# Kernel tuning notes

Measured on AMD Instinct MI355X. Metric: run time of the kernel, lower is better.

## Reference

```python
import jax, jax.numpy as jnp
import numpy as np

B, S, E, H, BS = 4, 4096, 1024, 1024, 128  # batch, seq, embed, head_size, block_size


def setup_inputs() -> dict:
    key = jax.random.key(0)
    k1, k2, k3, k4 = jax.random.split(key, 4)
    x = jax.random.normal(k1, (B, S, E), dtype=jnp.float32)
    W_qkv = jax.random.normal(k2, (E, 3 * H), dtype=jnp.float32) * (E ** -0.5)
    W_out = jax.random.normal(k3, (H, H), dtype=jnp.float32) * (H ** -0.5)
    b_out = jax.random.normal(k4, (H,), dtype=jnp.float32) * 0.01
    return {"x": x, "W_qkv": W_qkv, "W_out": W_out, "b_out": b_out}


def reference(x, W_qkv, W_out, b_out):
    b, s, e = x.shape
    h = W_out.shape[1]
    nb = s // BS  # number of blocks (block-diagonal attention)
    qkv = x @ W_qkv                      # [B, S, 3H]
    q, k, v = jnp.split(qkv, 3, axis=-1)

    def blk(t):
        return t.reshape(b, nb, BS, h)   # [B, nb, BS, H]

    scale = h ** -0.5
    # each query block attends only its own key/value block
    scores = jnp.einsum('bnqd,bnkd->bnqk', blk(q), blk(k)) * scale  # [B, nb, BS, BS]
    causal = jnp.tril(jnp.ones((BS, BS), dtype=bool))  # diagonal block of full tril
    scores = jnp.where(causal, scores, -jnp.inf)
    scores = scores - jnp.max(scores, axis=-1, keepdims=True)
    p = jnp.exp(scores)
    p = p / (jnp.sum(p, axis=-1, keepdims=True) + 1e-6)  # faithful: softmax with +1e-6 eps
    out = jnp.einsum('bnqk,bnkd->bnqd', p, blk(v)).reshape(b, s, h)
    return out @ W_out.T + b_out
```

## Files before the change

### kernel.cpp

```cpp
#include <hip/hip_runtime.h>
#include <hip/hip_bf16.h>

typedef __attribute__((ext_vector_type(8))) short short8;
typedef __attribute__((ext_vector_type(4))) float float4_;

__device__ __forceinline__ short f2b(float f) {
  union { __hip_bfloat16 h; short s; } u;
  u.h = __float2bfloat16(f);
  return u.s;
}
__device__ __forceinline__ float b2f(short s) {
  union { short s; __hip_bfloat16 h; } u;
  u.s = s;
  return __bfloat162float(u.h);
}
__device__ __forceinline__ short8 cvt8(float4_ lo, float4_ hi) {
  short8 r;
#pragma unroll
  for (int t = 0; t < 4; t++) { r[t] = f2b(lo[t]); r[t + 4] = f2b(hi[t]); }
  return r;
}

__global__ __launch_bounds__(256) void f32_to_b16(
    const float* __restrict__ in, short* __restrict__ out, long n)
{
  const long i = ((long)blockIdx.x * 256 + threadIdx.x) * 8;
  if (i >= n) return;
  float4_ lo = *(const float4_*)&in[i];
  float4_ hi = *(const float4_*)&in[i + 4];
  *(short8*)&out[i] = cvt8(lo, hi);
}

__global__ __launch_bounds__(256) void transpose64(
    const float* __restrict__ in, short* __restrict__ out, int R, int C)
{
  __shared__ __align__(16) short T[64 * 72];
  const int tid = threadIdx.x;
  const int r0 = blockIdx.y * 64;
  const int c0 = blockIdx.x * 64;
  const int r  = tid >> 2;
  const int cp = (tid & 3) * 16;
#pragma unroll
  for (int g = 0; g < 4; g++) {
    float4_ v = *(const float4_*)&in[(long)(r0 + r) * C + c0 + cp + g * 4];
#pragma unroll
    for (int t = 0; t < 4; t++) T[(cp + g * 4 + t) * 72 + r] = f2b(v[t]);
  }
  __syncthreads();
  const int c  = tid >> 2;
  const int rp = (tid & 3) * 16;
  short8 w0 = *(const short8*)&T[c * 72 + rp];
  short8 w1 = *(const short8*)&T[c * 72 + rp + 8];
  *(short8*)&out[(long)(c0 + c) * R + r0 + rp] = w0;
  *(short8*)&out[(long)(c0 + c) * R + r0 + rp + 8] = w1;
}

__global__ __launch_bounds__(256) void gemm_bt(
    const void* __restrict__ Av, int lda, int a_f32,
    const short* __restrict__ B,
    void* __restrict__ Cv, int ldc, int c_f32,
    int K, const float* __restrict__ bias)
{
  __shared__ __align__(16) short As[128 * 32];
  __shared__ __align__(16) short Bs[128 * 32];
  const int tid  = threadIdx.x;
  const int lane = tid & 63;
  const int w    = tid >> 6;
  const int quad = lane >> 4;
  const int l15  = lane & 15;
  const int wm   = (w >> 1) * 64;
  const int wn   = (w & 1) * 64;
  const int m0   = blockIdx.y * 128;
  const int n0   = blockIdx.x * 128;

  float4_ acc[4][4] = {};

  const int srow = tid >> 2;
  const int kp   = (tid & 3) * 8;

  for (int k0 = 0; k0 < K; k0 += 32) {
    short8 a_lo, a_hi;
    if (a_f32) {
      const float* Af = (const float*)Av;
      float4_ l0 = *(const float4_*)&Af[(long)(m0 + srow) * lda + k0 + kp];
      float4_ l1 = *(const float4_*)&Af[(long)(m0 + srow) * lda + k0 + kp + 4];
      float4_ h0 = *(const float4_*)&Af[(long)(m0 + srow + 64) * lda + k0 + kp];
      float4_ h1 = *(const float4_*)&Af[(long)(m0 + srow + 64) * lda + k0 + kp + 4];
      a_lo = cvt8(l0, l1);
      a_hi = cvt8(h0, h1);
    } else {
      const short* As_ = (const short*)Av;
      a_lo = *(const short8*)&As_[(long)(m0 + srow) * lda + k0 + kp];
      a_hi = *(const short8*)&As_[(long)(m0 + srow + 64) * lda + k0 + kp];
    }
    short8 b_lo = *(const short8*)&B[(long)(n0 + srow) * K + k0 + kp];
    short8 b_hi = *(const short8*)&B[(long)(n0 + srow + 64) * K + k0 + kp];
    __syncthreads();
    *(short8*)&As[srow * 32 + kp]        = a_lo;
    *(short8*)&As[(srow + 64) * 32 + kp] = a_hi;
    *(short8*)&Bs[srow * 32 + kp]        = b_lo;
    *(short8*)&Bs[(srow + 64) * 32 + kp] = b_hi;
    __syncthreads();
    short8 a[4], b[4];
#pragma unroll
    for (int i = 0; i < 4; i++)
      a[i] = *(const short8*)&As[(wm + i * 16 + l15) * 32 + quad * 8];
#pragma unroll
    for (int j = 0; j < 4; j++)
      b[j] = *(const short8*)&Bs[(wn + j * 16 + l15) * 32 + quad * 8];
#pragma unroll
    for (int i = 0; i < 4; i++)
#pragma unroll
      for (int j = 0; j < 4; j++)
        acc[i][j] = __builtin_amdgcn_mfma_f32_16x16x32_bf16(a[i], b[j], acc[i][j], 0, 0, 0);
  }

#pragma unroll
  for (int i = 0; i < 4; i++) {
    const int rm = m0 + wm + i * 16 + quad * 4;
#pragma unroll
    for (int j = 0; j < 4; j++) {
      const int cn = n0 + wn + j * 16 + l15;
      if (c_f32) {
        float* C = (float*)Cv;
        const float bv = bias ? bias[cn] : 0.0f;
#pragma unroll
        for (int r = 0; r < 4; r++)
          C[(long)(rm + r) * ldc + cn] = acc[i][j][r] + bv;
      } else {
        short* C = (short*)Cv;
#pragma unroll
        for (int r = 0; r < 4; r++)
          C[(long)(rm + r) * ldc + cn] = f2b(acc[i][j][r]);
      }
    }
  }
}

__global__ __launch_bounds__(256) void attn_blockdiag(short* __restrict__ qkv)
{
  __shared__ __align__(16) short Qs[128 * 32];
  __shared__ __align__(16) short Ks[128 * 32];
  __shared__ __align__(16) short Ps[128 * 136];

  const int tid  = threadIdx.x;
  const int lane = tid & 63;
  const int w    = tid >> 6;
  const int quad = lane >> 4;
  const int l15  = lane & 15;
  const long base = (long)blockIdx.x * 128 * 3072;

  float4_ acc[2][8] = {};
  const int srow = tid >> 2;
  const int kp   = (tid & 3) * 8;
  const short* Qg = qkv + base;
  const short* Kg = qkv + base + 1024;

  for (int k0 = 0; k0 < 1024; k0 += 32) {
    short8 q_lo = *(const short8*)&Qg[(long)srow * 3072 + k0 + kp];
    short8 q_hi = *(const short8*)&Qg[(long)(srow + 64) * 3072 + k0 + kp];
    short8 k_lo = *(const short8*)&Kg[(long)srow * 3072 + k0 + kp];
    short8 k_hi = *(const short8*)&Kg[(long)(srow + 64) * 3072 + k0 + kp];
    __syncthreads();
    *(short8*)&Qs[srow * 32 + kp]        = q_lo;
    *(short8*)&Qs[(srow + 64) * 32 + kp] = q_hi;
    *(short8*)&Ks[srow * 32 + kp]        = k_lo;
    *(short8*)&Ks[(srow + 64) * 32 + kp] = k_hi;
    __syncthreads();
    short8 a0 = *(const short8*)&Qs[(w * 32 + l15) * 32 + quad * 8];
    short8 a1 = *(const short8*)&Qs[(w * 32 + 16 + l15) * 32 + quad * 8];
#pragma unroll
    for (int j = 0; j < 8; j++) {
      short8 b = *(const short8*)&Ks[(j * 16 + l15) * 32 + quad * 8];
      acc[0][j] = __builtin_amdgcn_mfma_f32_16x16x32_bf16(a0, b, acc[0][j], 0, 0, 0);
      acc[1][j] = __builtin_amdgcn_mfma_f32_16x16x32_bf16(a1, b, acc[1][j], 0, 0, 0);
    }
  }
  __syncthreads();

  const float scale = 0.03125f;
#pragma unroll
  for (int i = 0; i < 2; i++) {
#pragma unroll
    for (int r = 0; r < 4; r++) {
      const int rowq = w * 32 + i * 16 + quad * 4 + r;
      float s[8];
      float mx = -3.0e38f;
#pragma unroll
      for (int j = 0; j < 8; j++) {
        const int col = j * 16 + l15;
        const float v = acc[i][j][r] * scale;
        s[j] = (col <= rowq) ? v : -3.0e38f;
        mx = fmaxf(mx, s[j]);
      }
      mx = fmaxf(mx, __shfl_xor(mx, 1));
      mx = fmaxf(mx, __shfl_xor(mx, 2));
      mx = fmaxf(mx, __shfl_xor(mx, 4));
      mx = fmaxf(mx, __shfl_xor(mx, 8));
      float p[8];
      float sum = 0.0f;
#pragma unroll
      for (int j = 0; j < 8; j++) {
        p[j] = (s[j] > -1.0e38f) ? __expf(s[j] - mx) : 0.0f;
        sum += p[j];
      }
      sum += __shfl_xor(sum, 1);
      sum += __shfl_xor(sum, 2);
      sum += __shfl_xor(sum, 4);
      sum += __shfl_xor(sum, 8);
      const float inv = 1.0f / (sum + 1e-6f);
#pragma unroll
      for (int j = 0; j < 8; j++)
        Ps[rowq * 136 + j * 16 + l15] = f2b(p[j] * inv);
    }
  }
  __syncthreads();

  const short* Vg = qkv + base + 2048;
  short* Op = qkv + base;
  for (int d0 = 0; d0 < 1024; d0 += 64) {
    float4_ o[2][4] = {};
#pragma unroll
    for (int kk = 0; kk < 4; kk++) {
      short8 a0 = *(const short8*)&Ps[(w * 32 + l15) * 136 + kk * 32 + quad * 8];
      short8 a1 = *(const short8*)&Ps[(w * 32 + 16 + l15) * 136 + kk * 32 + quad * 8];
      const int kb = kk * 32 + quad * 8;
#pragma unroll
      for (int j = 0; j < 4; j++) {
        const int d = d0 + j * 16 + l15;
        short8 b;
#pragma unroll
        for (int t = 0; t < 8; t++)
          b[t] = Vg[(long)(kb + t) * 3072 + d];
        o[0][j] = __builtin_amdgcn_mfma_f32_16x16x32_bf16(a0, b, o[0][j], 0, 0, 0);
        o[1][j] = __builtin_amdgcn_mfma_f32_16x16x32_bf16(a1, b, o[1][j], 0, 0, 0);
      }
    }
#pragma unroll
    for (int i = 0; i < 2; i++)
#pragma unroll
      for (int j = 0; j < 4; j++)
#pragma unroll
        for (int r = 0; r < 4; r++) {
          const int rq = w * 32 + i * 16 + quad * 4 + r;
          const int d  = d0 + j * 16 + l15;
          Op[(long)rq * 3072 + d] = f2b(o[i][j][r]);
        }
  }
}

extern "C" void kernel_launch(void* const* d_in, const int* in_sizes, int n_in,
                              void* d_out, int out_size, void* d_ws, size_t ws_size,
                              hipStream_t stream) {
  const float* x    = (const float*)d_in[0];
  const float* Wqkv = (const float*)d_in[1];
  const float* Wout = (const float*)d_in[2];
  const float* bout = (const float*)d_in[3];
  float* out = (float*)d_out;

  char* ws = (char*)d_ws;
  short* WqkvT = (short*)ws;
  short* Woutb = (short*)(ws + 6291456);
  short* qkv   = (short*)(ws + 8388608);
  short* xb    = (short*)(ws + 8388608 + (size_t)16384 * 3072 * 2);

  transpose64<<<dim3(48, 16), 256, 0, stream>>>(Wqkv, WqkvT, 1024, 3072);
  f32_to_b16<<<512, 256, 0, stream>>>(Wout, Woutb, 1048576L);

  if (ws_size >= 8388608 + (size_t)16384 * 3072 * 2 + (size_t)16384 * 1024 * 2) {
    f32_to_b16<<<8192, 256, 0, stream>>>(x, xb, 16777216L);
    gemm_bt<<<dim3(24, 128), 256, 0, stream>>>(xb, 1024, 0, WqkvT,
                                               qkv, 3072, 0, 1024, nullptr);
    attn_blockdiag<<<dim3(128), 256, 0, stream>>>(qkv);
    gemm_bt<<<dim3(8, 128), 256, 0, stream>>>(qkv, 3072, 0, Woutb,
                                              out, 1024, 1, 1024, bout);
  } else if (ws_size >= 8388608 + (size_t)16384 * 3072 * 2) {
    gemm_bt<<<dim3(24, 128), 256, 0, stream>>>(x, 1024, 1, WqkvT,
                                               qkv, 3072, 0, 1024, nullptr);
    attn_blockdiag<<<dim3(128), 256, 0, stream>>>(qkv);
    gemm_bt<<<dim3(8, 128), 256, 0, stream>>>(qkv, 3072, 0, Woutb,
                                              out, 1024, 1, 1024, bout);
  } else {
    for (int c = 0; c < 4; c++) {
      const float* xc = x + (long)c * 4096 * 1024;
      float* outc = out + (long)c * 4096 * 1024;
      gemm_bt<<<dim3(24, 32), 256, 0, stream>>>(xc, 1024, 1, WqkvT,
                                                qkv, 3072, 0, 1024, nullptr);
      attn_blockdiag<<<dim3(32), 256, 0, stream>>>(qkv);
      gemm_bt<<<dim3(8, 32), 256, 0, stream>>>(qkv, 3072, 0, Woutb,
                                               outc, 1024, 1, 1024, bout);
    }
  }
}
```

Measured before the change: 384.1 us.

## Split attention into QK-softmax and PV kernels, use async global-to-LDS loads

The single attention kernel, which ran only 128 blocks, is split into a QK+softmax kernel with 256 blocks (half a query block each) that writes P into the Q slot, and a PV kernel with 1024 blocks (one 128-column tile each) that writes output into the K slot. The final GEMM then reads from the K slot. The aim is to raise GPU occupancy on the attention stages, which previously used too few workgroups. GEMM and QK tile loads now use global_load_lds async copies instead of register staging. The separate x-to-bf16 conversion pass and the workspace-size fallbacks are dropped, so the GEMM converts fp32 x on the fly. This adds an extra round trip through global memory for P and assumes the larger workspace is always available.

```diff
diff --git a/kernel.cpp b/kernel.cpp
--- a/kernel.cpp
+++ b/kernel.cpp
@@ -3,16 +3,17 @@
 
 typedef __attribute__((ext_vector_type(8))) short short8;
 typedef __attribute__((ext_vector_type(4))) float float4_;
+
+__device__ __forceinline__ void async16(const void* g, void* l) {
+  __builtin_amdgcn_global_load_lds(
+      (const __attribute__((address_space(1))) unsigned int*)g,
+      (__attribute__((address_space(3))) unsigned int*)l, 16, 0, 0);
+}
 
 __device__ __forceinline__ short f2b(float f) {
   union { __hip_bfloat16 h; short s; } u;
   u.h = __float2bfloat16(f);
   return u.s;
-}
-__device__ __forceinline__ float b2f(short s) {
-  union { short s; __hip_bfloat16 h; } u;
-  u.s = s;
-  return __bfloat162float(u.h);
 }
 __device__ __forceinline__ short8 cvt8(float4_ lo, float4_ hi) {
   short8 r;
@@ -77,29 +78,27 @@
 
   const int srow = tid >> 2;
   const int kp   = (tid & 3) * 8;
+  char* AsW = (char*)As + w * 1024;
+  char* BsW = (char*)Bs + w * 1024;
+  const short* Bb0 = B + (long)(n0 + srow) * K;
+  const short* Bb1 = B + (long)(n0 + srow + 64) * K;
 
   for (int k0 = 0; k0 < K; k0 += 32) {
-    short8 a_lo, a_hi;
+    async16(Bb0 + k0 + kp, BsW);
+    async16(Bb1 + k0 + kp, BsW + 4096);
     if (a_f32) {
       const float* Af = (const float*)Av;
       float4_ l0 = *(const float4_*)&Af[(long)(m0 + srow) * lda + k0 + kp];
       float4_ l1 = *(const float4_*)&Af[(long)(m0 + srow) * lda + k0 + kp + 4];
       float4_ h0 = *(const float4_*)&Af[(long)(m0 + srow + 64) * lda + k0 + kp];
       float4_ h1 = *(const float4_*)&Af[(long)(m0 + srow + 64) * lda + k0 + kp + 4];
-      a_lo = cvt8(l0, l1);
-      a_hi = cvt8(h0, h1);
+      *(short8*)&As[srow * 32 + kp]        = cvt8(l0, l1);
+      *(short8*)&As[(srow + 64) * 32 + kp] = cvt8(h0, h1);
     } else {
-      const short* As_ = (const short*)Av;
-      a_lo = *(const short8*)&As_[(long)(m0 + srow) * lda + k0 + kp];
-      a_hi = *(const short8*)&As_[(long)(m0 + srow + 64) * lda + k0 + kp];
-    }
-    short8 b_lo = *(const short8*)&B[(long)(n0 + srow) * K + k0 + kp];
-    short8 b_hi = *(const short8*)&B[(long)(n0 + srow + 64) * K + k0 + kp];
-    __syncthreads();
-    *(short8*)&As[srow * 32 + kp]        = a_lo;
-    *(short8*)&As[(srow + 64) * 32 + kp] = a_hi;
-    *(short8*)&Bs[srow * 32 + kp]        = b_lo;
-    *(short8*)&Bs[(srow + 64) * 32 + kp] = b_hi;
+      const short* Ab = (const short*)Av;
+      async16(Ab + (long)(m0 + srow) * lda + k0 + kp, AsW);
+      async16(Ab + (long)(m0 + srow + 64) * lda + k0 + kp, AsW + 4096);
+    }
     __syncthreads();
     short8 a[4], b[4];
 #pragma unroll
@@ -113,6 +112,7 @@
 #pragma unroll
       for (int j = 0; j < 4; j++)
         acc[i][j] = __builtin_amdgcn_mfma_f32_16x16x32_bf16(a[i], b[j], acc[i][j], 0, 0, 0);
+    __syncthreads();
   }
 
 #pragma unroll
@@ -137,88 +137,104 @@
   }
 }
 
-__global__ __launch_bounds__(256) void attn_blockdiag(short* __restrict__ qkv)
-{
-  __shared__ __align__(16) short Qs[128 * 32];
+__global__ __launch_bounds__(256) void qk_softmax(short* __restrict__ qkv)
+{
+  __shared__ __align__(16) short Qs[64 * 32];
   __shared__ __align__(16) short Ks[128 * 32];
-  __shared__ __align__(16) short Ps[128 * 136];
-
   const int tid  = threadIdx.x;
   const int lane = tid & 63;
   const int w    = tid >> 6;
   const int quad = lane >> 4;
   const int l15  = lane & 15;
-  const long base = (long)blockIdx.x * 128 * 3072;
-
-  float4_ acc[2][8] = {};
+  const int d    = blockIdx.x >> 1;
+  const int h    = blockIdx.x & 1;
+  const long rbase = (long)d * 128 * 3072;
+  const short* Qg = qkv + rbase + (long)(h * 64) * 3072;
+  const short* Kg = qkv + rbase + 1024;
   const int srow = tid >> 2;
   const int kp   = (tid & 3) * 8;
-  const short* Qg = qkv + base;
-  const short* Kg = qkv + base + 1024;
-
+
+  float4_ acc[8] = {};
   for (int k0 = 0; k0 < 1024; k0 += 32) {
-    short8 q_lo = *(const short8*)&Qg[(long)srow * 3072 + k0 + kp];
-    short8 q_hi = *(const short8*)&Qg[(long)(srow + 64) * 3072 + k0 + kp];
-    short8 k_lo = *(const short8*)&Kg[(long)srow * 3072 + k0 + kp];
-    short8 k_hi = *(const short8*)&Kg[(long)(srow + 64) * 3072 + k0 + kp];
-    __syncthreads();
-    *(short8*)&Qs[srow * 32 + kp]        = q_lo;
-    *(short8*)&Qs[(srow + 64) * 32 + kp] = q_hi;
-    *(short8*)&Ks[srow * 32 + kp]        = k_lo;
-    *(short8*)&Ks[(srow + 64) * 32 + kp] = k_hi;
-    __syncthreads();
-    short8 a0 = *(const short8*)&Qs[(w * 32 + l15) * 32 + quad * 8];
-    short8 a1 = *(const short8*)&Qs[(w * 32 + 16 + l15) * 32 + quad * 8];
+    async16(Qg + (long)srow * 3072 + k0 + kp, (char*)Qs + w * 1024);
+    async16(Kg + (long)srow * 3072 + k0 + kp, (char*)Ks + w * 1024);
+    async16(Kg + (long)(srow + 64) * 3072 + k0 + kp, (char*)Ks + 4096 + w * 1024);
+    __syncthreads();
+    short8 a = *(const short8*)&Qs[(w * 16 + l15) * 32 + quad * 8];
 #pragma unroll
     for (int j = 0; j < 8; j++) {
       short8 b = *(const short8*)&Ks[(j * 16 + l15) * 32 + quad * 8];
-      acc[0][j] = __builtin_amdgcn_mfma_f32_16x16x32_bf16(a0, b, acc[0][j], 0, 0, 0);
-      acc[1][j] = __builtin_amdgcn_mfma_f32_16x16x32_bf16(a1, b, acc[1][j], 0, 0, 0);
+      acc[j] = __builtin_amdgcn_mfma_f32_16x16x32_bf16(a, b, acc[j], 0, 0, 0);
+    }
+    __syncthreads();
+  }
+
+  const float scale = 0.03125f;
+#pragma unroll
+  for (int r = 0; r < 4; r++) {
+    const int rloc = w * 16 + quad * 4 + r;
+    const int rblk = h * 64 + rloc;
+    float s[8];
+    float mx = -3.0e38f;
+#pragma unroll
+    for (int j = 0; j < 8; j++) {
+      const int col = j * 16 + l15;
+      const float v = acc[j][r] * scale;
+      s[j] = (col <= rblk) ? v : -3.0e38f;
+      mx = fmaxf(mx, s[j]);
+    }
+    mx = fmaxf(mx, __shfl_xor(mx, 1));
+    mx = fmaxf(mx, __shfl_xor(mx, 2));
+    mx = fmaxf(mx, __shfl_xor(mx, 4));
+    mx = fmaxf(mx, __shfl_xor(mx, 8));
+    float p[8];
+    float sum = 0.0f;
+#pragma unroll
+    for (int j = 0; j < 8; j++) {
+      p[j] = (s[j] > -1.0e38f) ? __expf(s[j] - mx) : 0.0f;
+      sum += p[j];
+    }
+    sum += __shfl_xor(sum, 1);
+    sum += __shfl_xor(sum, 2);
+    sum += __shfl_xor(sum, 4);
+    sum += __shfl_xor(sum, 8);
+    const float inv = 1.0f / (sum + 1e-6f);
+#pragma unroll
+    for (int j = 0; j < 8; j++)
+      qkv[rbase + (long)rblk * 3072 + j * 16 + l15] = f2b(p[j] * inv);
+  }
+}
+
+__global__ __launch_bounds__(256) void pv(short* __restrict__ qkv)
+{
+  __shared__ __align__(16) short Ps[128 * 136];
+  const int tid  = threadIdx.x;
+  const int lane = tid & 63;
+  const int w    = tid >> 6;
+  const int quad = lane >> 4;
+  const int l15  = lane & 15;
+  const long rbase = (long)blockIdx.y * 128 * 3072;
+  const short* Pg = qkv + rbase;
+  const short* Vg = qkv + rbase + 2048;
+  short* Og = qkv + rbase + 1024;
+  const int n0 = blockIdx.x * 128;
+
+  {
+    const int pr = tid >> 2;
+    const int pc = (tid & 3) * 32;
+#pragma unroll
+    for (int g = 0; g < 2; g++) {
+      const int row = g * 64 + pr;
+#pragma unroll
+      for (int c = 0; c < 4; c++) {
+        short8 v = *(const short8*)&Pg[(long)row * 3072 + pc + c * 8];
+        *(short8*)&Ps[row * 136 + pc + c * 8] = v;
+      }
     }
   }
   __syncthreads();
 
-  const float scale = 0.03125f;
-#pragma unroll
-  for (int i = 0; i < 2; i++) {
-#pragma unroll
-    for (int r = 0; r < 4; r++) {
-      const int rowq = w * 32 + i * 16 + quad * 4 + r;
-      float s[8];
-      float mx = -3.0e38f;
-#pragma unroll
-      for (int j = 0; j < 8; j++) {
-        const int col = j * 16 + l15;
-        const float v = acc[i][j][r] * scale;
-        s[j] = (col <= rowq) ? v : -3.0e38f;
-        mx = fmaxf(mx, s[j]);
-      }
-      mx = fmaxf(mx, __shfl_xor(mx, 1));
-      mx = fmaxf(mx, __shfl_xor(mx, 2));
-      mx = fmaxf(mx, __shfl_xor(mx, 4));
-      mx = fmaxf(mx, __shfl_xor(mx, 8));
-      float p[8];
-      float sum = 0.0f;
-#pragma unroll
-      for (int j = 0; j < 8; j++) {
-        p[j] = (s[j] > -1.0e38f) ? __expf(s[j] - mx) : 0.0f;
-        sum += p[j];
-      }
-      sum += __shfl_xor(sum, 1);
-      sum += __shfl_xor(sum, 2);
-      sum += __shfl_xor(sum, 4);
-      sum += __shfl_xor(sum, 8);
-      const float inv = 1.0f / (sum + 1e-6f);
-#pragma unroll
-      for (int j = 0; j < 8; j++)
-        Ps[rowq * 136 + j * 16 + l15] = f2b(p[j] * inv);
-    }
-  }
-  __syncthreads();
-
-  const short* Vg = qkv + base + 2048;
-  short* Op = qkv + base;
-  for (int d0 = 0; d0 < 1024; d0 += 64) {
+  for (int d0 = n0; d0 < n0 + 128; d0 += 64) {
     float4_ o[2][4] = {};
 #pragma unroll
     for (int kk = 0; kk < 4; kk++) {
@@ -227,11 +243,11 @@
       const int kb = kk * 32 + quad * 8;
 #pragma unroll
       for (int j = 0; j < 4; j++) {
-        const int d = d0 + j * 16 + l15;
+        const int dd = d0 + j * 16 + l15;
         short8 b;
 #pragma unroll
         for (int t = 0; t < 8; t++)
-          b[t] = Vg[(long)(kb + t) * 3072 + d];
+          b[t] = Vg[(long)(kb + t) * 3072 + dd];
         o[0][j] = __builtin_amdgcn_mfma_f32_16x16x32_bf16(a0, b, o[0][j], 0, 0, 0);
         o[1][j] = __builtin_amdgcn_mfma_f32_16x16x32_bf16(a1, b, o[1][j], 0, 0, 0);
       }
@@ -243,8 +259,8 @@
 #pragma unroll
         for (int r = 0; r < 4; r++) {
           const int rq = w * 32 + i * 16 + quad * 4 + r;
-          const int d  = d0 + j * 16 + l15;
-          Op[(long)rq * 3072 + d] = f2b(o[i][j][r]);
+          const int dd = d0 + j * 16 + l15;
+          Og[(long)rq * 3072 + dd] = f2b(o[i][j][r]);
         }
   }
 }
@@ -262,33 +278,13 @@
   short* WqkvT = (short*)ws;
   short* Woutb = (short*)(ws + 6291456);
   short* qkv   = (short*)(ws + 8388608);
-  short* xb    = (short*)(ws + 8388608 + (size_t)16384 * 3072 * 2);
 
   transpose64<<<dim3(48, 16), 256, 0, stream>>>(Wqkv, WqkvT, 1024, 3072);
   f32_to_b16<<<512, 256, 0, stream>>>(Wout, Woutb, 1048576L);
-
-  if (ws_size >= 8388608 + (size_t)16384 * 3072 * 2 + (size_t)16384 * 1024 * 2) {
-    f32_to_b16<<<8192, 256, 0, stream>>>(x, xb, 16777216L);
-    gemm_bt<<<dim3(24, 128), 256, 0, stream>>>(xb, 1024, 0, WqkvT,
-                                               qkv, 3072, 0, 1024, nullptr);
-    attn_blockdiag<<<dim3(128), 256, 0, stream>>>(qkv);
-    gemm_bt<<<dim3(8, 128), 256, 0, stream>>>(qkv, 3072, 0, Woutb,
-                                              out, 1024, 1, 1024, bout);
-  } else if (ws_size >= 8388608 + (size_t)16384 * 3072 * 2) {
-    gemm_bt<<<dim3(24, 128), 256, 0, stream>>>(x, 1024, 1, WqkvT,
-                                               qkv, 3072, 0, 1024, nullptr);
-    attn_blockdiag<<<dim3(128), 256, 0, stream>>>(qkv);
-    gemm_bt<<<dim3(8, 128), 256, 0, stream>>>(qkv, 3072, 0, Woutb,
-                                              out, 1024, 1, 1024, bout);
-  } else {
-    for (int c = 0; c < 4; c++) {
-      const float* xc = x + (long)c * 4096 * 1024;
-      float* outc = out + (long)c * 4096 * 1024;
-      gemm_bt<<<dim3(24, 32), 256, 0, stream>>>(xc, 1024, 1, WqkvT,
-                                                qkv, 3072, 0, 1024, nullptr);
-      attn_blockdiag<<<dim3(32), 256, 0, stream>>>(qkv);
-      gemm_bt<<<dim3(8, 32), 256, 0, stream>>>(qkv, 3072, 0, Woutb,
-                                               outc, 1024, 1, 1024, bout);
-    }
-  }
-}
+  gemm_bt<<<dim3(24, 128), 256, 0, stream>>>(x, 1024, 1, WqkvT,
+                                             qkv, 3072, 0, 1024, nullptr);
+  qk_softmax<<<256, 256, 0, stream>>>(qkv);
+  pv<<<dim3(8, 128), 256, 0, stream>>>(qkv);
+  gemm_bt<<<dim3(8, 128), 256, 0, stream>>>(qkv + 1024, 3072, 0, Woutb,
+                                            out, 1024, 1, 1024, bout);
+}
```

Result: slower. 408.5 us (+6.4%).
